# Performance work log

Hardware: AMD Instinct MI355X
Metric: run time of the kernel (lower is better)

The kernel has to match this reference:

```python
import jax, jax.numpy as jnp
import numpy as np

BETA_MIN = 0.1
BETA_MAX = 20.0


def _Beta(t):
    # integral of linear beta schedule
    return BETA_MIN * t + 0.5 * (BETA_MAX - BETA_MIN) * t ** 2


def setup_inputs() -> dict:
    key = jax.random.key(0)
    k1, k2, k3, k4, k5 = jax.random.split(key, 5)
    B, K, D = 4096, 128, 256
    x = jax.random.normal(k1, (B, D), dtype=jnp.float32)
    t = jax.random.uniform(k2, (B,), dtype=jnp.float32)
    centers = jax.random.normal(k3, (K, D), dtype=jnp.float32)
    # keep stds positive and well-conditioned
    stds = 0.5 + 0.5 * jax.random.uniform(k4, (K, D), dtype=jnp.float32)
    # positive mixture weights (original only requires positivity, takes log)
    weights = 0.1 + jax.random.uniform(k5, (K,), dtype=jnp.float32)
    return {"x": x, "t": t, "centers": centers, "stds": stds, "weights": weights}


def reference(x, t, centers, stds, weights):
    ndim = centers.shape[1]

    def log_prob(xx):
        Bt = _Beta(t)[:, None, None]                 # [B,1,1]
        a = jnp.exp(-Bt / 2)
        centers_t = a * centers[None]                # [B,K,D]
        var_t = jnp.exp(-Bt) * stds[None] ** 2 + 1.0 - jnp.exp(-Bt)  # [B,K,D]
        diff = xx[:, None, :] - centers_t            # [B,K,D]
        # NOTE: faithful to source, which uses ndim/2 * sum(log(2*pi*var)) (not 1/2)
        lp = (-(diff ** 2) / (2.0 * var_t)).sum(-1) \
             - (ndim / 2) * jnp.log(2.0 * jnp.pi * var_t).sum(-1)    # [B,K]
        lp = lp + jnp.log(weights)[None, :]
        return jax.scipy.special.logsumexp(lp, axis=1)               # [B]

    grad_log_prob = jax.grad(lambda xx: log_prob(xx).sum())(x)       # [B,D]
    Bt = _Beta(t)[:, None]                                           # [B,1]
    return -jnp.sqrt(1.0 - jnp.exp(-Bt)) * grad_log_prob
```

## Files before the change

kernel.cpp:

```cpp
#include <hip/hip_runtime.h>
#include <math.h>


constexpr int Kc = 128;
constexpr int Dc = 256;
constexpr int G  = 4;

typedef float f2 __attribute__((ext_vector_type(2)));
typedef float f4 __attribute__((ext_vector_type(4)));

static __device__ __forceinline__ f2 fma2(f2 a, f2 b, f2 c) {
    return __builtin_elementwise_fma(a, b, c);
}
static __device__ __forceinline__ f2 splat2(float s) { return (f2){s, s}; }

__global__ void prep_kernel(const float* __restrict__ centers,
                            const float* __restrict__ stds,
                            float* __restrict__ CA8, f2* __restrict__ P2) {
    int idx = blockIdx.x * blockDim.x + threadIdx.x;
    if (idx >= Kc * Dc) return;
    int k = idx >> 8;
    int d = idx & (Dc - 1);
    float c = centers[idx];
    float s = stds[idx];
    float A = s * s - 1.0f;
    int o = (d >> 2) * (Kc * 8) + k * 8 + (d & 3);
    CA8[o]     = c;
    CA8[o + 4] = A;
    P2[idx] = (f2){c, A};
}

__global__ __launch_bounds__(256, 6) void score_kernel(
    const float* __restrict__ x, const float* __restrict__ t,
    const float* __restrict__ weights,
    const float* __restrict__ CA8, const f2* __restrict__ P2,
    float* __restrict__ out)
{
    const int b0  = blockIdx.x * G;
    const int tid = threadIdx.x;

    __shared__ __align__(16) float xT[Dc][G];
    __shared__ float part1[G][2][Kc];
    __shared__ float partL[G][2][Kc];
    __shared__ __align__(16) float peT[Kc][G];
    __shared__ float wmax[G][2];
    __shared__ float wsum[G][2];

    float e[G], na[G], sg[G];
    #pragma unroll
    for (int g = 0; g < G; ++g) {
        float tt = t[b0 + g];
        float Bt = fmaf(9.95f * tt, tt, 0.1f * tt);
        float ee = __expf(-Bt);
        e[g]  = ee;
        na[g] = -sqrtf(ee);
        sg[g] = sqrtf(1.0f - ee);
    }
    f2 e2[2]  = {{e[0], e[1]}, {e[2], e[3]}};
    f2 na2[2] = {{na[0], na[1]}, {na[2], na[3]}};
    const f2 one2 = {1.0f, 1.0f};

    #pragma unroll
    for (int g = 0; g < G; ++g)
        xT[tid][g] = x[(b0 + g) * Dc + tid];
    __syncthreads();

    const int kk    = tid & (Kc - 1);
    const int half  = tid >> 7;
    const int dbase = half * (Dc / 2);

    const f4* xTv = (const f4*)(&xT[0][0]);

    f2 acc1[2] = {{0.f, 0.f}, {0.f, 0.f}};
    float accL[G] = {0.f, 0.f, 0.f, 0.f};

    for (int grp = 0; grp < 8; ++grp) {
        f2 prod[2] = {{1.f, 1.f}, {1.f, 1.f}};
        #pragma unroll
        for (int q = 0; q < 4; ++q) {
            const int d0 = dbase + (grp * 4 + q) * 4;
            const float* base = CA8 + ((size_t)(d0 >> 2) * Kc + kk) * 8;
            f4 c4 = *(const f4*)base;
            f4 A4 = *(const f4*)(base + 4);
            f4 xv0 = xTv[d0 + 0];
            f4 xv1 = xTv[d0 + 1];
            f4 xv2 = xTv[d0 + 2];
            f4 xv3 = xTv[d0 + 3];
            #pragma unroll
            for (int p = 0; p < 2; ++p) {
                f2 ep = e2[p], nap = na2[p];
                f2 x0 = {xv0[2*p], xv0[2*p+1]};
                f2 x1 = {xv1[2*p], xv1[2*p+1]};
                f2 x2 = {xv2[2*p], xv2[2*p+1]};
                f2 x3 = {xv3[2*p], xv3[2*p+1]};
                f2 v0 = fma2(ep, splat2(A4[0]), one2);
                f2 v1 = fma2(ep, splat2(A4[1]), one2);
                f2 v2 = fma2(ep, splat2(A4[2]), one2);
                f2 v3 = fma2(ep, splat2(A4[3]), one2);
                f2 f0 = fma2(nap, splat2(c4[0]), x0);
                f2 f1 = fma2(nap, splat2(c4[1]), x1);
                f2 f2_ = fma2(nap, splat2(c4[2]), x2);
                f2 f3 = fma2(nap, splat2(c4[3]), x3);
                f2 s0 = f0 * f0, s1 = f1 * f1, s2 = f2_ * f2_, s3 = f3 * f3;
                f2 d01 = v0 * v1, d23 = v2 * v3;
                f2 n01 = fma2(s1, v0, s0 * v1);
                f2 n23 = fma2(s3, v2, s2 * v3);
                f2 den = d01 * d23;
                f2 num = fma2(n23, d01, n01 * d23);
                f2 r = {__builtin_amdgcn_rcpf(den[0]),
                        __builtin_amdgcn_rcpf(den[1])};
                acc1[p] = fma2(num, r, acc1[p]);
                prod[p] = prod[p] * den;
            }
        }
        accL[0] += __log2f(prod[0][0]);
        accL[1] += __log2f(prod[0][1]);
        accL[2] += __log2f(prod[1][0]);
        accL[3] += __log2f(prod[1][1]);
    }
    #pragma unroll
    for (int p = 0; p < 2; ++p) {
        part1[2*p  ][half][kk] = acc1[p][0];
        part1[2*p+1][half][kk] = acc1[p][1];
    }
    #pragma unroll
    for (int g = 0; g < G; ++g)
        partL[g][half][kk] = accL[g];
    __syncthreads();

    float lpv[G];
    if (tid < Kc) {
        float lw = __logf(weights[tid]);
        #pragma unroll
        for (int g = 0; g < G; ++g) {
            float S1 = part1[g][0][tid] + part1[g][1][tid];
            float S2 = partL[g][0][tid] + partL[g][1][tid];
            lpv[g] = fmaf(-0.5f, S1, fmaf(-88.72283911167299f, S2, lw));
            float m = lpv[g];
            #pragma unroll
            for (int off = 32; off > 0; off >>= 1)
                m = fmaxf(m, __shfl_xor(m, off, 64));
            if ((tid & 63) == 0) wmax[g][tid >> 6] = m;
        }
    }
    __syncthreads();
    if (tid < Kc) {
        #pragma unroll
        for (int g = 0; g < G; ++g) {
            float m  = fmaxf(wmax[g][0], wmax[g][1]);
            float pe = __expf(lpv[g] - m);
            peT[tid][g] = pe;
            float s = pe;
            #pragma unroll
            for (int off = 32; off > 0; off >>= 1)
                s += __shfl_xor(s, off, 64);
            if ((tid & 63) == 0) wsum[g][tid >> 6] = s;
        }
    }
    __syncthreads();

    f4 xvv = xTv[tid];
    f2 xp[2] = {{xvv[0], xvv[1]}, {xvv[2], xvv[3]}};
    f2 O[2] = {{0.f, 0.f}, {0.f, 0.f}};
    const f4* peTv = (const f4*)(&peT[0][0]);
    const f2* pp = P2 + tid;

    for (int kq = 0; kq < 32; ++kq) {
        const int k0 = kq * 4;
        f2 ca0 = pp[(k0 + 0) * Dc];
        f2 ca1 = pp[(k0 + 1) * Dc];
        f2 ca2 = pp[(k0 + 2) * Dc];
        f2 ca3 = pp[(k0 + 3) * Dc];
        f4 p0 = peTv[k0 + 0];
        f4 p1 = peTv[k0 + 1];
        f4 p2 = peTv[k0 + 2];
        f4 p3 = peTv[k0 + 3];
        #pragma unroll
        for (int p = 0; p < 2; ++p) {
            f2 ep = e2[p], nap = na2[p];
            f2 v0 = fma2(ep, splat2(ca0[1]), one2);
            f2 v1 = fma2(ep, splat2(ca1[1]), one2);
            f2 v2 = fma2(ep, splat2(ca2[1]), one2);
            f2 v3 = fma2(ep, splat2(ca3[1]), one2);
            f2 f0 = fma2(nap, splat2(ca0[0]), xp[p]);
            f2 f1 = fma2(nap, splat2(ca1[0]), xp[p]);
            f2 f2_ = fma2(nap, splat2(ca2[0]), xp[p]);
            f2 f3 = fma2(nap, splat2(ca3[0]), xp[p]);
            f2 u0 = (f2){p0[2*p], p0[2*p+1]} * f0;
            f2 u1 = (f2){p1[2*p], p1[2*p+1]} * f1;
            f2 u2 = (f2){p2[2*p], p2[2*p+1]} * f2_;
            f2 u3 = (f2){p3[2*p], p3[2*p+1]} * f3;
            f2 d01 = v0 * v1, d23 = v2 * v3;
            f2 n01 = fma2(u1, v0, u0 * v1);
            f2 n23 = fma2(u3, v2, u2 * v3);
            f2 den = d01 * d23;
            f2 num = fma2(n23, d01, n01 * d23);
            f2 r = {__builtin_amdgcn_rcpf(den[0]),
                    __builtin_amdgcn_rcpf(den[1])};
            O[p] = fma2(num, r, O[p]);
        }
    }

    #pragma unroll
    for (int p = 0; p < 2; ++p) {
        #pragma unroll
        for (int j = 0; j < 2; ++j) {
            int g = 2 * p + j;
            float Z = wsum[g][0] + wsum[g][1];
            out[(b0 + g) * Dc + tid] = sg[g] * __builtin_amdgcn_rcpf(Z) * O[p][j];
        }
    }
}

extern "C" void kernel_launch(void* const* d_in, const int* in_sizes, int n_in,
                              void* d_out, int out_size, void* d_ws, size_t ws_size,
                              hipStream_t stream) {
    const float* x       = (const float*)d_in[0];
    const float* t       = (const float*)d_in[1];
    const float* centers = (const float*)d_in[2];
    const float* stds    = (const float*)d_in[3];
    const float* weights = (const float*)d_in[4];
    float* outp = (float*)d_out;

    float* CA8 = (float*)d_ws;
    f2*    P2  = (f2*)(CA8 + Kc * Dc * 2);

    const int B = in_sizes[1];

    prep_kernel<<<(Kc * Dc + 255) / 256, 256, 0, stream>>>(centers, stds, CA8, P2);
    score_kernel<<<B / G, 256, 0, stream>>>(x, t, weights, CA8, P2, outp);
}
```

Measured before the change: 102.3 us.

## Double block size to 512 threads and split D and K loops across more threads

```diff
diff --git a/kernel.cpp b/kernel.cpp
--- a/kernel.cpp
+++ b/kernel.cpp
@@ -30,7 +30,7 @@
     P2[idx] = (f2){c, A};
 }
 
-__global__ __launch_bounds__(256, 6) void score_kernel(
+__global__ __launch_bounds__(512, 8) void score_kernel(
     const float* __restrict__ x, const float* __restrict__ t,
     const float* __restrict__ weights,
     const float* __restrict__ CA8, const f2* __restrict__ P2,
@@ -40,11 +40,12 @@
     const int tid = threadIdx.x;
 
     __shared__ __align__(16) float xT[Dc][G];
-    __shared__ float part1[G][2][Kc];
-    __shared__ float partL[G][2][Kc];
+    __shared__ float part1[G][4][Kc];
+    __shared__ float partL[G][4][Kc];
     __shared__ __align__(16) float peT[Kc][G];
     __shared__ float wmax[G][2];
     __shared__ float wsum[G][2];
+    __shared__ __align__(16) float Opart[G][Dc];
 
     float e[G], na[G], sg[G];
     #pragma unroll
@@ -60,21 +61,24 @@
     f2 na2[2] = {{na[0], na[1]}, {na[2], na[3]}};
     const f2 one2 = {1.0f, 1.0f};
 
-    #pragma unroll
-    for (int g = 0; g < G; ++g)
-        xT[tid][g] = x[(b0 + g) * Dc + tid];
-    __syncthreads();
-
-    const int kk    = tid & (Kc - 1);
-    const int half  = tid >> 7;
-    const int dbase = half * (Dc / 2);
+    {
+        const int dd = tid & (Dc - 1);
+        const int gh = tid >> 8;
+        xT[dd][gh]     = x[(b0 + gh) * Dc + dd];
+        xT[dd][gh + 2] = x[(b0 + gh + 2) * Dc + dd];
+    }
+    __syncthreads();
+
+    const int kk      = tid & (Kc - 1);
+    const int quarter = tid >> 7;
+    const int dbase   = quarter * (Dc / 4);
 
     const f4* xTv = (const f4*)(&xT[0][0]);
 
     f2 acc1[2] = {{0.f, 0.f}, {0.f, 0.f}};
     float accL[G] = {0.f, 0.f, 0.f, 0.f};
 
-    for (int grp = 0; grp < 8; ++grp) {
+    for (int grp = 0; grp < 4; ++grp) {
         f2 prod[2] = {{1.f, 1.f}, {1.f, 1.f}};
         #pragma unroll
         for (int q = 0; q < 4; ++q) {
@@ -120,12 +124,12 @@
     }
     #pragma unroll
     for (int p = 0; p < 2; ++p) {
-        part1[2*p  ][half][kk] = acc1[p][0];
-        part1[2*p+1][half][kk] = acc1[p][1];
+        part1[2*p  ][quarter][kk] = acc1[p][0];
+        part1[2*p+1][quarter][kk] = acc1[p][1];
     }
     #pragma unroll
     for (int g = 0; g < G; ++g)
-        partL[g][half][kk] = accL[g];
+        partL[g][quarter][kk] = accL[g];
     __syncthreads();
 
     float lpv[G];
@@ -133,8 +137,10 @@
         float lw = __logf(weights[tid]);
         #pragma unroll
         for (int g = 0; g < G; ++g) {
-            float S1 = part1[g][0][tid] + part1[g][1][tid];
-            float S2 = partL[g][0][tid] + partL[g][1][tid];
+            float S1 = (part1[g][0][tid] + part1[g][1][tid])
+                     + (part1[g][2][tid] + part1[g][3][tid]);
+            float S2 = (partL[g][0][tid] + partL[g][1][tid])
+                     + (partL[g][2][tid] + partL[g][3][tid]);
             lpv[g] = fmaf(-0.5f, S1, fmaf(-88.72283911167299f, S2, lw));
             float m = lpv[g];
             #pragma unroll
@@ -159,13 +165,16 @@
     }
     __syncthreads();
 
-    f4 xvv = xTv[tid];
+    const int dd    = tid & (Dc - 1);
+    const int khalf = tid >> 8;
+    f4 xvv = xTv[dd];
     f2 xp[2] = {{xvv[0], xvv[1]}, {xvv[2], xvv[3]}};
     f2 O[2] = {{0.f, 0.f}, {0.f, 0.f}};
     const f4* peTv = (const f4*)(&peT[0][0]);
-    const f2* pp = P2 + tid;
-
-    for (int kq = 0; kq < 32; ++kq) {
+    const f2* pp = P2 + dd;
+
+    const int kq0 = khalf * 16;
+    for (int kq = kq0; kq < kq0 + 16; ++kq) {
         const int k0 = kq * 4;
         f2 ca0 = pp[(k0 + 0) * Dc];
         f2 ca1 = pp[(k0 + 1) * Dc];
@@ -201,13 +210,25 @@
         }
     }
 
-    #pragma unroll
-    for (int p = 0; p < 2; ++p) {
-        #pragma unroll
-        for (int j = 0; j < 2; ++j) {
-            int g = 2 * p + j;
-            float Z = wsum[g][0] + wsum[g][1];
-            out[(b0 + g) * Dc + tid] = sg[g] * __builtin_amdgcn_rcpf(Z) * O[p][j];
+    if (khalf) {
+        #pragma unroll
+        for (int p = 0; p < 2; ++p) {
+            #pragma unroll
+            for (int j = 0; j < 2; ++j)
+                Opart[2*p + j][dd] = O[p][j];
+        }
+    }
+    __syncthreads();
+    if (!khalf) {
+        #pragma unroll
+        for (int p = 0; p < 2; ++p) {
+            #pragma unroll
+            for (int j = 0; j < 2; ++j) {
+                int g = 2 * p + j;
+                float Z  = wsum[g][0] + wsum[g][1];
+                float Ov = O[p][j] + Opart[g][dd];
+                out[(b0 + g) * Dc + dd] = sg[g] * __builtin_amdgcn_rcpf(Z) * Ov;
+            }
         }
     }
 }
@@ -228,5 +249,5 @@
     const int B = in_sizes[1];
 
     prep_kernel<<<(Kc * Dc + 255) / 256, 256, 0, stream>>>(centers, stds, CA8, P2);
-    score_kernel<<<B / G, 256, 0, stream>>>(x, t, weights, CA8, P2, outp);
-}
+    score_kernel<<<B / G, 512, 0, stream>>>(x, t, weights, CA8, P2, outp);
+}
```

Result: slower. 105.3 us (+3.0%).
